# Optimization experiments

Hardware: AMD Instinct MI355X
Metric: run time of the kernel (lower is better)

Reference implementation:

```python
import jax, jax.numpy as jnp
import numpy as np

N_NODES = 50000
N_EDGES = 1600000
D_IN = 512
D_OUT = 512


def setup_inputs() -> dict:
    key = jax.random.key(0)
    ks = jax.random.split(key, 10)
    x = jax.random.normal(ks[0], (N_NODES, D_IN), dtype=jnp.float32)
    w0 = jax.random.normal(ks[1], (D_IN, D_OUT), dtype=jnp.float32) * 0.02
    w1 = jax.random.normal(ks[2], (D_IN, D_OUT), dtype=jnp.float32) * 0.02
    b = jax.random.normal(ks[3], (D_OUT,), dtype=jnp.float32) * 0.02
    vals0 = jax.random.uniform(ks[4], (N_EDGES,), dtype=jnp.float32)
    vals1 = jax.random.uniform(ks[5], (N_EDGES,), dtype=jnp.float32)
    rows0 = jax.random.randint(ks[6], (N_EDGES,), 0, N_NODES, dtype=jnp.int32)
    cols0 = jax.random.randint(ks[7], (N_EDGES,), 0, N_NODES, dtype=jnp.int32)
    rows1 = jax.random.randint(ks[8], (N_EDGES,), 0, N_NODES, dtype=jnp.int32)
    cols1 = jax.random.randint(ks[9], (N_EDGES,), 0, N_NODES, dtype=jnp.int32)
    return {"x": x, "w0": w0, "w1": w1, "b": b,
            "vals0": vals0, "vals1": vals1,
            "rows0": rows0, "cols0": cols0, "rows1": rows1, "cols1": cols1}


def _spmm(rows, cols, vals, dense):
    # sparse [N,N] @ dense [N,D]: gather source rows, scale, scatter-add to dest rows
    gathered = vals[:, None] * dense[cols]  # [E, D]
    return jax.ops.segment_sum(gathered, rows, num_segments=N_NODES)


def reference(x, w0, w1, b, vals0, vals1, rows0, cols0, rows1, cols1):
    # dropout rate is 0.0 (dropout=False), so input passes through unchanged
    pre0 = x @ w0  # [N, D_out]
    pre1 = x @ w1
    s0 = _spmm(rows0, cols0, vals0, pre0)
    s1 = _spmm(rows1, cols1, vals1, pre1)
    out = s0 + s1 + b  # add_n over supports, then bias
    return jax.nn.relu(out)
```

## Files before the change

### kernel.cpp

```cpp
#include <hip/hip_runtime.h>
#include <cstdint>
#include <cstddef>

#define N_NODES 50000
#define N_EDGES 1600000
#define D 512
#define MPAD 50048
#define NPX 6250
#define CAP 80
#define TILE_SHIFT 11
#define NTILES 25

typedef __attribute__((ext_vector_type(8))) short bf16x8;
typedef __attribute__((ext_vector_type(4))) float f32x4;
typedef __attribute__((ext_vector_type(8))) unsigned short u16x8;
typedef __attribute__((ext_vector_type(4))) int i32x4;

static __device__ __forceinline__ unsigned short f2bf(float f) {
  unsigned u = __float_as_uint(f);
  u += 0x7fffu + ((u >> 16) & 1u);
  return (unsigned short)(u >> 16);
}

__global__ __launch_bounds__(256) void prep(const float* __restrict__ x,
                                            const float* __restrict__ w0,
                                            const float* __restrict__ w1,
                                            signed char* __restrict__ xq,
                                            float* __restrict__ scale,
                                            unsigned short* __restrict__ wbT,
                                            int* __restrict__ cnt) {
  __shared__ float ts[64][68];
  const int t = threadIdx.x;
  if (blockIdx.x < 12500) {
    const int lane = t & 63;
    const int wave = t >> 6;
    const int n = blockIdx.x * 4 + wave;
    const float* xr = x + (size_t)n * D + lane * 8;
    f32x4 f0 = __builtin_nontemporal_load((const f32x4*)xr);
    f32x4 f1 = __builtin_nontemporal_load((const f32x4*)xr + 1);
    float m = fmaxf(fmaxf(fmaxf(fabsf(f0[0]), fabsf(f0[1])), fmaxf(fabsf(f0[2]), fabsf(f0[3]))),
                    fmaxf(fmaxf(fabsf(f1[0]), fabsf(f1[1])), fmaxf(fabsf(f1[2]), fabsf(f1[3]))));
    #pragma unroll
    for (int off = 32; off >= 1; off >>= 1) m = fmaxf(m, __shfl_xor(m, off, 64));
    m = fmaxf(m, 1e-20f);
    const float inv = 127.0f / m;
    int q[8];
    q[0] = (int)rintf(f0[0] * inv); q[1] = (int)rintf(f0[1] * inv);
    q[2] = (int)rintf(f0[2] * inv); q[3] = (int)rintf(f0[3] * inv);
    q[4] = (int)rintf(f1[0] * inv); q[5] = (int)rintf(f1[1] * inv);
    q[6] = (int)rintf(f1[2] * inv); q[7] = (int)rintf(f1[3] * inv);
    unsigned lo = (q[0] & 0xff) | ((q[1] & 0xff) << 8) | ((q[2] & 0xff) << 16) | ((unsigned)(q[3] & 0xff) << 24);
    unsigned hi = (q[4] & 0xff) | ((q[5] & 0xff) << 8) | ((q[6] & 0xff) << 16) | ((unsigned)(q[7] & 0xff) << 24);
    *(uint2*)(xq + (size_t)n * D + lane * 8) = make_uint2(lo, hi);
    if (lane == 0) scale[n] = m * (1.0f / 127.0f);
  } else if (blockIdx.x < 12628) {
    const int bid2 = blockIdx.x - 12500;
    const int m = bid2 >> 6;
    const int tile = bid2 & 63;
    const int k0 = (tile >> 3) * 64;
    const int j0 = (tile & 7) * 64;
    const float* W = m ? w1 : w0;
    const int tr = t >> 4;
    const int tc = (t & 15) * 4;
    #pragma unroll
    for (int it = 0; it < 4; ++it) {
      int kk = tr + it * 16;
      float4 v = *(const float4*)&W[(size_t)(k0 + kk) * 512 + j0 + tc];
      ts[kk][tc] = v.x; ts[kk][tc + 1] = v.y; ts[kk][tc + 2] = v.z; ts[kk][tc + 3] = v.w;
    }
    __syncthreads();
    const int jl = t >> 3;
    const int kl = (t & 7) * 8;
    #pragma unroll
    for (int it = 0; it < 2; ++it) {
      int j = jl + it * 32;
      u16x8 o;
      #pragma unroll
      for (int q2 = 0; q2 < 8; ++q2) o[q2] = f2bf(ts[kl + q2][j]);
      *(u16x8*)&wbT[(size_t)(j0 + j) * 1024 + m * 512 + k0 + kl] = o;
    }
  } else {
    int q2 = (int)(blockIdx.x - 12628) * 256 + t;
    if (q2 < 25000) ((i32x4*)cnt)[q2] = (i32x4)0;
  }
}

__global__ __launch_bounds__(256) void fill_bucket(
    const int* __restrict__ r0, const int* __restrict__ co0, const float* __restrict__ v0,
    const int* __restrict__ r1, const int* __restrict__ co1, const float* __restrict__ v1,
    const float* __restrict__ scale,
    int* __restrict__ cnt0, int* __restrict__ cnt1,
    unsigned* __restrict__ e0, unsigned* __restrict__ e1) {
  const int nq = N_EDGES / 4;
  const int lo = (int)(blockIdx.x & 7) * NPX;
  const int hi = lo + NPX;
  const int stride = (1024 >> 3) * 256;
  for (int i = (int)(blockIdx.x >> 3) * 256 + threadIdx.x; i < 2 * nq; i += stride) {
    if (i < nq) {
      i32x4 r = ((const i32x4*)r0)[i];
      i32x4 c = ((const i32x4*)co0)[i];
      f32x4 v = ((const f32x4*)v0)[i];
      #pragma unroll
      for (int k = 0; k < 4; ++k) {
        if (r[k] >= lo && r[k] < hi) {
          int slot = atomicAdd(&cnt0[r[k]], 1);
          if (slot < CAP)
            e0[(size_t)r[k] * CAP + slot] =
                (unsigned)c[k] | ((unsigned)f2bf(v[k] * scale[c[k]]) << 16);
        }
      }
    } else {
      int j = i - nq;
      i32x4 r = ((const i32x4*)r1)[j];
      i32x4 c = ((const i32x4*)co1)[j];
      f32x4 v = ((const f32x4*)v1)[j];
      #pragma unroll
      for (int k = 0; k < 4; ++k) {
        if (r[k] >= lo && r[k] < hi) {
          int slot = atomicAdd(&cnt1[r[k]], 1);
          if (slot < CAP)
            e1[(size_t)r[k] * CAP + slot] =
                (unsigned)c[k] | ((unsigned)f2bf(v[k] * scale[c[k]]) << 16);
        }
      }
    }
  }
}

static __device__ __forceinline__ void acc8(float* a, uint2 q, float v) {
  #pragma unroll
  for (int i = 0; i < 4; ++i) {
    a[i]     += v * (float)(signed char)(q.x >> (8 * i));
    a[i + 4] += v * (float)(signed char)(q.y >> (8 * i));
  }
}

__global__ __launch_bounds__(256) void spmm_sorted(const signed char* __restrict__ xq,
    const int* __restrict__ cnt0, const unsigned* __restrict__ e0,
    const int* __restrict__ cnt1, const unsigned* __restrict__ e1,
    unsigned short* __restrict__ s) {
  __shared__ unsigned sed[4][2][CAP];
  __shared__ int cur[4][2][NTILES];
  __shared__ unsigned short starts[4][2][NTILES + 1];
  const int t = threadIdx.x;
  const int lane = t & 63;
  const int wave = t >> 6;
  const int n = blockIdx.x * 4 + wave;
  const int c0 = lane * 8;

  int deg0 = cnt0[n]; if (deg0 > CAP) deg0 = CAP;
  int deg1 = cnt1[n]; if (deg1 > CAP) deg1 = CAP;
  const unsigned* eb0 = e0 + (size_t)n * CAP;
  const unsigned* eb1 = e1 + (size_t)n * CAP;

  for (int b = lane; b < 2 * NTILES; b += 64) ((int*)cur[wave])[b] = 0;
  __syncthreads();

  unsigned my0[2] = {0u, 0u}, my1[2] = {0u, 0u};
  #pragma unroll
  for (int q = 0; q < 2; ++q) {
    int p = lane + q * 64;
    if (p < deg0) {
      unsigned m = eb0[p]; my0[q] = m;
      atomicAdd(&cur[wave][0][(m & 0xffffu) >> TILE_SHIFT], 1);
    }
    if (p < deg1) {
      unsigned m = eb1[p]; my1[q] = m;
      atomicAdd(&cur[wave][1][(m & 0xffffu) >> TILE_SHIFT], 1);
    }
  }
  __syncthreads();

  if (lane < 2) {
    int acc2 = 0;
    for (int t2 = 0; t2 < NTILES; ++t2) {
      starts[wave][lane][t2] = (unsigned short)acc2;
      int h = cur[wave][lane][t2];
      cur[wave][lane][t2] = acc2;
      acc2 += h;
    }
    starts[wave][lane][NTILES] = (unsigned short)acc2;
  }
  __syncthreads();

  #pragma unroll
  for (int q = 0; q < 2; ++q) {
    int p = lane + q * 64;
    if (p < deg0) {
      unsigned m = my0[q];
      int pos = atomicAdd(&cur[wave][0][(m & 0xffffu) >> TILE_SHIFT], 1);
      sed[wave][0][pos] = m;
    }
    if (p < deg1) {
      unsigned m = my1[q];
      int pos = atomicAdd(&cur[wave][1][(m & 0xffffu) >> TILE_SHIFT], 1);
      sed[wave][1][pos] = m;
    }
  }
  __syncthreads();

  float acc[2][8] = {};
  for (int t2 = 0; t2 < NTILES; ++t2) {
    #pragma unroll
    for (int sup = 0; sup < 2; ++sup) {
      float* a = acc[sup];
      int p = starts[wave][sup][t2];
      const int pe = starts[wave][sup][t2 + 1];
      for (; p + 1 < pe; p += 2) {
        unsigned mA = sed[wave][sup][p];
        unsigned mB = sed[wave][sup][p + 1];
        uint2 qA = *(const uint2*)(xq + (size_t)(mA & 0xffffu) * D + c0);
        uint2 qB = *(const uint2*)(xq + (size_t)(mB & 0xffffu) * D + c0);
        float vA = __uint_as_float(mA & 0xffff0000u);
        float vB = __uint_as_float(mB & 0xffff0000u);
        acc8(a, qA, vA);
        acc8(a, qB, vB);
      }
      if (p < pe) {
        unsigned m = sed[wave][sup][p];
        uint2 q = *(const uint2*)(xq + (size_t)(m & 0xffffu) * D + c0);
        float v = __uint_as_float(m & 0xffff0000u);
        acc8(a, q, v);
      }
    }
  }

  u16x8 o0, o1;
  #pragma unroll
  for (int i = 0; i < 8; ++i) { o0[i] = f2bf(acc[0][i]); o1[i] = f2bf(acc[1][i]); }
  *(u16x8*)(s + (size_t)n * 1024 + c0) = o0;
  *(u16x8*)(s + (size_t)n * 1024 + 512 + c0) = o1;
}

#define BM 128
#define BN 256
#define BK 32

__global__ __launch_bounds__(256) void gemm_out(const unsigned short* __restrict__ s,
                                                const unsigned short* __restrict__ wbT,
                                                const float* __restrict__ bias,
                                                float* __restrict__ out) {
  __shared__ __align__(16) unsigned short As[2][BM * BK];
  __shared__ __align__(16) unsigned short Bs[2][BN * BK];
  const int t = threadIdx.x;
  const int lane = t & 63;
  const int wave = t >> 6;
  const int wm = wave >> 1, wn = wave & 1;
  const int lr = lane & 15;
  const int slot = lane >> 4;
  const int m0 = blockIdx.y * BM;
  const int n0 = blockIdx.x * BN;

  f32x4 acc[4][8] = {};
  const int NT = 1024 / BK;

  auto STAGE = [&](int buf, int kt) {
    #pragma unroll
    for (int i = 0; i < 2; ++i) {
      int ch = i * 256 + t;
      int row = ch >> 2;
      int sl = ch & 3;
      int ke = (sl ^ ((row >> 1) & 3)) * 8;
      const unsigned short* ga = s + (size_t)(m0 + row) * 1024 + kt * BK + ke;
      __builtin_amdgcn_global_load_lds(
          (const __attribute__((address_space(1))) unsigned int*)ga,
          (__attribute__((address_space(3))) unsigned int*)(&As[buf][ch * 8]), 16, 0, 0);
    }
    #pragma unroll
    for (int i = 0; i < 4; ++i) {
      int ch = i * 256 + t;
      int row = ch >> 2;
      int sl = ch & 3;
      int ke = (sl ^ ((row >> 1) & 3)) * 8;
      const unsigned short* gb = wbT + (size_t)(n0 + row) * 1024 + kt * BK + ke;
      __builtin_amdgcn_global_load_lds(
          (const __attribute__((address_space(1))) unsigned int*)gb,
          (__attribute__((address_space(3))) unsigned int*)(&Bs[buf][ch * 8]), 16, 0, 0);
    }
  };

  STAGE(0, 0);
  __syncthreads();

  for (int kt = 0; kt < NT; ++kt) {
    const int cur = kt & 1;
    if (kt + 1 < NT) STAGE(cur ^ 1, kt + 1);

    bf16x8 a[4], b[8];
    #pragma unroll
    for (int i = 0; i < 4; ++i) {
      int row = wm * 64 + i * 16 + lr;
      a[i] = *(const bf16x8*)&As[cur][row * BK + (slot ^ ((row >> 1) & 3)) * 8];
    }
    #pragma unroll
    for (int j = 0; j < 8; ++j) {
      int row = wn * 128 + j * 16 + lr;
      b[j] = *(const bf16x8*)&Bs[cur][row * BK + (slot ^ ((row >> 1) & 3)) * 8];
    }
    #pragma unroll
    for (int i = 0; i < 4; ++i)
      #pragma unroll
      for (int j = 0; j < 8; ++j)
        acc[i][j] = __builtin_amdgcn_mfma_f32_16x16x32_bf16(a[i], b[j], acc[i][j], 0, 0, 0);
    __syncthreads();
  }

  float bj[8];
  #pragma unroll
  for (int j = 0; j < 8; ++j) bj[j] = bias[n0 + wn * 128 + j * 16 + lr];

  const int orow = slot * 4;
  #pragma unroll
  for (int i = 0; i < 4; ++i) {
    #pragma unroll
    for (int j = 0; j < 8; ++j) {
      #pragma unroll
      for (int r = 0; r < 4; ++r) {
        int row = m0 + wm * 64 + i * 16 + orow + r;
        if (row < N_NODES) {
          int col = n0 + wn * 128 + j * 16 + lr;
          __builtin_nontemporal_store(fmaxf(acc[i][j][r] + bj[j], 0.f),
                                      out + (size_t)row * 512 + col);
        }
      }
    }
  }
}

extern "C" void kernel_launch(void* const* d_in, const int* in_sizes, int n_in,
                              void* d_out, int out_size, void* d_ws, size_t ws_size,
                              hipStream_t stream) {
  const float* x     = (const float*)d_in[0];
  const float* w0    = (const float*)d_in[1];
  const float* w1    = (const float*)d_in[2];
  const float* bias  = (const float*)d_in[3];
  const float* vals0 = (const float*)d_in[4];
  const float* vals1 = (const float*)d_in[5];
  const int*   rows0 = (const int*)d_in[6];
  const int*   cols0 = (const int*)d_in[7];
  const int*   rows1 = (const int*)d_in[8];
  const int*   cols1 = (const int*)d_in[9];
  float* out = (float*)d_out;

  char* ws = (char*)d_ws;
  size_t off = 0;
  auto alloc = [&](size_t bytes) -> char* {
    char* p = ws + off;
    off += (bytes + 255) & ~(size_t)255;
    return p;
  };
  signed char*    xq    = (signed char*)alloc((size_t)N_NODES * D);
  float*          scale = (float*)alloc((size_t)N_NODES * sizeof(float));
  unsigned short* wbT   = (unsigned short*)alloc((size_t)512 * 1024 * 2);
  unsigned short* s     = (unsigned short*)alloc((size_t)MPAD * 1024 * 2);
  int* cnt  = (int*)alloc(2 * N_NODES * sizeof(int));
  unsigned* e0 = (unsigned*)alloc((size_t)N_NODES * CAP * 4);
  unsigned* e1 = (unsigned*)alloc((size_t)N_NODES * CAP * 4);

  prep<<<12726, 256, 0, stream>>>(x, w0, w1, xq, scale, wbT, cnt);
  fill_bucket<<<1024, 256, 0, stream>>>(rows0, cols0, vals0, rows1, cols1, vals1,
                                        scale, cnt, cnt + N_NODES, e0, e1);
  spmm_sorted<<<N_NODES / 4, 256, 0, stream>>>(xq, cnt, e0, cnt + N_NODES, e1, s);
  gemm_out<<<dim3(512 / BN, MPAD / BM), 256, 0, stream>>>(s, wbT, bias, out);
}
```

Baseline: 503.7 us.

## Use offset-unsigned int8 quantization in SpMM and retile output GEMM to full width

```diff
diff --git a/kernel.cpp b/kernel.cpp
--- a/kernel.cpp
+++ b/kernel.cpp
@@ -25,7 +25,7 @@
 __global__ __launch_bounds__(256) void prep(const float* __restrict__ x,
                                             const float* __restrict__ w0,
                                             const float* __restrict__ w1,
-                                            signed char* __restrict__ xq,
+                                            unsigned char* __restrict__ xq,
                                             float* __restrict__ scale,
                                             unsigned short* __restrict__ wbT,
                                             int* __restrict__ cnt) {
@@ -45,10 +45,10 @@
     m = fmaxf(m, 1e-20f);
     const float inv = 127.0f / m;
     int q[8];
-    q[0] = (int)rintf(f0[0] * inv); q[1] = (int)rintf(f0[1] * inv);
-    q[2] = (int)rintf(f0[2] * inv); q[3] = (int)rintf(f0[3] * inv);
-    q[4] = (int)rintf(f1[0] * inv); q[5] = (int)rintf(f1[1] * inv);
-    q[6] = (int)rintf(f1[2] * inv); q[7] = (int)rintf(f1[3] * inv);
+    q[0] = (int)rintf(f0[0] * inv) + 128; q[1] = (int)rintf(f0[1] * inv) + 128;
+    q[2] = (int)rintf(f0[2] * inv) + 128; q[3] = (int)rintf(f0[3] * inv) + 128;
+    q[4] = (int)rintf(f1[0] * inv) + 128; q[5] = (int)rintf(f1[1] * inv) + 128;
+    q[6] = (int)rintf(f1[2] * inv) + 128; q[7] = (int)rintf(f1[3] * inv) + 128;
     unsigned lo = (q[0] & 0xff) | ((q[1] & 0xff) << 8) | ((q[2] & 0xff) << 16) | ((unsigned)(q[3] & 0xff) << 24);
     unsigned hi = (q[4] & 0xff) | ((q[5] & 0xff) << 8) | ((q[6] & 0xff) << 16) | ((unsigned)(q[7] & 0xff) << 24);
     *(uint2*)(xq + (size_t)n * D + lane * 8) = make_uint2(lo, hi);
@@ -127,15 +127,18 @@
   }
 }
 
-static __device__ __forceinline__ void acc8(float* a, uint2 q, float v) {
-  #pragma unroll
-  for (int i = 0; i < 4; ++i) {
-    a[i]     += v * (float)(signed char)(q.x >> (8 * i));
-    a[i + 4] += v * (float)(signed char)(q.y >> (8 * i));
-  }
-}
-
-__global__ __launch_bounds__(256) void spmm_sorted(const signed char* __restrict__ xq,
+static __device__ __forceinline__ void acc8u(float* a, uint2 q, float v) {
+  a[0] += v * (float)(q.x & 0xffu);
+  a[1] += v * (float)((q.x >> 8) & 0xffu);
+  a[2] += v * (float)((q.x >> 16) & 0xffu);
+  a[3] += v * (float)((q.x >> 24) & 0xffu);
+  a[4] += v * (float)(q.y & 0xffu);
+  a[5] += v * (float)((q.y >> 8) & 0xffu);
+  a[6] += v * (float)((q.y >> 16) & 0xffu);
+  a[7] += v * (float)((q.y >> 24) & 0xffu);
+}
+
+__global__ __launch_bounds__(256) void spmm_sorted(const unsigned char* __restrict__ xq,
     const int* __restrict__ cnt0, const unsigned* __restrict__ e0,
     const int* __restrict__ cnt1, const unsigned* __restrict__ e1,
     unsigned short* __restrict__ s) {
@@ -200,10 +203,12 @@
   __syncthreads();
 
   float acc[2][8] = {};
+  float sumv[2] = {0.f, 0.f};
   for (int t2 = 0; t2 < NTILES; ++t2) {
     #pragma unroll
     for (int sup = 0; sup < 2; ++sup) {
       float* a = acc[sup];
+      float sv = 0.f;
       int p = starts[wave][sup][t2];
       const int pe = starts[wave][sup][t2 + 1];
       for (; p + 1 < pe; p += 2) {
@@ -213,27 +218,33 @@
         uint2 qB = *(const uint2*)(xq + (size_t)(mB & 0xffffu) * D + c0);
         float vA = __uint_as_float(mA & 0xffff0000u);
         float vB = __uint_as_float(mB & 0xffff0000u);
-        acc8(a, qA, vA);
-        acc8(a, qB, vB);
+        acc8u(a, qA, vA);
+        acc8u(a, qB, vB);
+        sv += vA + vB;
       }
       if (p < pe) {
         unsigned m = sed[wave][sup][p];
         uint2 q = *(const uint2*)(xq + (size_t)(m & 0xffffu) * D + c0);
         float v = __uint_as_float(m & 0xffff0000u);
-        acc8(a, q, v);
-      }
+        acc8u(a, q, v);
+        sv += v;
+      }
+      sumv[sup] += sv;
     }
   }
 
   u16x8 o0, o1;
   #pragma unroll
-  for (int i = 0; i < 8; ++i) { o0[i] = f2bf(acc[0][i]); o1[i] = f2bf(acc[1][i]); }
+  for (int i = 0; i < 8; ++i) {
+    o0[i] = f2bf(acc[0][i] - 128.0f * sumv[0]);
+    o1[i] = f2bf(acc[1][i] - 128.0f * sumv[1]);
+  }
   *(u16x8*)(s + (size_t)n * 1024 + c0) = o0;
   *(u16x8*)(s + (size_t)n * 1024 + 512 + c0) = o1;
 }
 
-#define BM 128
-#define BN 256
+#define BM 64
+#define BN 512
 #define BK 32
 
 __global__ __launch_bounds__(256) void gemm_out(const unsigned short* __restrict__ s,
@@ -248,16 +259,14 @@
   const int wm = wave >> 1, wn = wave & 1;
   const int lr = lane & 15;
   const int slot = lane >> 4;
-  const int m0 = blockIdx.y * BM;
-  const int n0 = blockIdx.x * BN;
-
-  f32x4 acc[4][8] = {};
+  const int m0 = blockIdx.x * BM;
+
+  f32x4 acc[2][16] = {};
   const int NT = 1024 / BK;
 
   auto STAGE = [&](int buf, int kt) {
-    #pragma unroll
-    for (int i = 0; i < 2; ++i) {
-      int ch = i * 256 + t;
+    {
+      int ch = t;
       int row = ch >> 2;
       int sl = ch & 3;
       int ke = (sl ^ ((row >> 1) & 3)) * 8;
@@ -267,12 +276,12 @@
           (__attribute__((address_space(3))) unsigned int*)(&As[buf][ch * 8]), 16, 0, 0);
     }
     #pragma unroll
-    for (int i = 0; i < 4; ++i) {
+    for (int i = 0; i < 8; ++i) {
       int ch = i * 256 + t;
       int row = ch >> 2;
       int sl = ch & 3;
       int ke = (sl ^ ((row >> 1) & 3)) * 8;
-      const unsigned short* gb = wbT + (size_t)(n0 + row) * 1024 + kt * BK + ke;
+      const unsigned short* gb = wbT + (size_t)row * 1024 + kt * BK + ke;
       __builtin_amdgcn_global_load_lds(
           (const __attribute__((address_space(1))) unsigned int*)gb,
           (__attribute__((address_space(3))) unsigned int*)(&Bs[buf][ch * 8]), 16, 0, 0);
@@ -286,39 +295,36 @@
     const int cur = kt & 1;
     if (kt + 1 < NT) STAGE(cur ^ 1, kt + 1);
 
-    bf16x8 a[4], b[8];
-    #pragma unroll
-    for (int i = 0; i < 4; ++i) {
-      int row = wm * 64 + i * 16 + lr;
+    bf16x8 a[2];
+    #pragma unroll
+    for (int i = 0; i < 2; ++i) {
+      int row = wm * 32 + i * 16 + lr;
       a[i] = *(const bf16x8*)&As[cur][row * BK + (slot ^ ((row >> 1) & 3)) * 8];
     }
     #pragma unroll
-    for (int j = 0; j < 8; ++j) {
-      int row = wn * 128 + j * 16 + lr;
-      b[j] = *(const bf16x8*)&Bs[cur][row * BK + (slot ^ ((row >> 1) & 3)) * 8];
-    }
-    #pragma unroll
-    for (int i = 0; i < 4; ++i)
-      #pragma unroll
-      for (int j = 0; j < 8; ++j)
-        acc[i][j] = __builtin_amdgcn_mfma_f32_16x16x32_bf16(a[i], b[j], acc[i][j], 0, 0, 0);
+    for (int j = 0; j < 16; ++j) {
+      int row = wn * 256 + j * 16 + lr;
+      bf16x8 b = *(const bf16x8*)&Bs[cur][row * BK + (slot ^ ((row >> 1) & 3)) * 8];
+      acc[0][j] = __builtin_amdgcn_mfma_f32_16x16x32_bf16(a[0], b, acc[0][j], 0, 0, 0);
+      acc[1][j] = __builtin_amdgcn_mfma_f32_16x16x32_bf16(a[1], b, acc[1][j], 0, 0, 0);
+    }
     __syncthreads();
   }
 
-  float bj[8];
-  #pragma unroll
-  for (int j = 0; j < 8; ++j) bj[j] = bias[n0 + wn * 128 + j * 16 + lr];
+  float bj[16];
+  #pragma unroll
+  for (int j = 0; j < 16; ++j) bj[j] = bias[wn * 256 + j * 16 + lr];
 
   const int orow = slot * 4;
   #pragma unroll
-  for (int i = 0; i < 4; ++i) {
-    #pragma unroll
-    for (int j = 0; j < 8; ++j) {
+  for (int i = 0; i < 2; ++i) {
+    #pragma unroll
+    for (int j = 0; j < 16; ++j) {
       #pragma unroll
       for (int r = 0; r < 4; ++r) {
-        int row = m0 + wm * 64 + i * 16 + orow + r;
+        int row = m0 + wm * 32 + i * 16 + orow + r;
         if (row < N_NODES) {
-          int col = n0 + wn * 128 + j * 16 + lr;
+          int col = wn * 256 + j * 16 + lr;
           __builtin_nontemporal_store(fmaxf(acc[i][j][r] + bj[j], 0.f),
                                       out + (size_t)row * 512 + col);
         }
@@ -349,7 +355,7 @@
     off += (bytes + 255) & ~(size_t)255;
     return p;
   };
-  signed char*    xq    = (signed char*)alloc((size_t)N_NODES * D);
+  unsigned char*  xq    = (unsigned char*)alloc((size_t)N_NODES * D);
   float*          scale = (float*)alloc((size_t)N_NODES * sizeof(float));
   unsigned short* wbT   = (unsigned short*)alloc((size_t)512 * 1024 * 2);
   unsigned short* s     = (unsigned short*)alloc((size_t)MPAD * 1024 * 2);
@@ -361,5 +367,5 @@
   fill_bucket<<<1024, 256, 0, stream>>>(rows0, cols0, vals0, rows1, cols1, vals1,
                                         scale, cnt, cnt + N_NODES, e0, e1);
   spmm_sorted<<<N_NODES / 4, 256, 0, stream>>>(xq, cnt, e0, cnt + N_NODES, e1, s);
-  gemm_out<<<dim3(512 / BN, MPAD / BM), 256, 0, stream>>>(s, wbT, bias, out);
-}
+  gemm_out<<<MPAD / BM, 256, 0, stream>>>(s, wbT, bias, out);
+}
```

After: 589.5 us. 17.0% more time.
